# Kernel optimization log

Hardware: AMD Instinct MI355X
Metric: run time of the kernel (lower is better)

The kernel has to match this reference:

```python
import jax, jax.numpy as jnp
import numpy as np

N = 300000; E = N - 1; A = 150000; D = 64; H = 128; T = 512
NEG_SLOPE = 0.2


def _gatv2(h, src, dst, Wl, bl, Wr, br, att, bias):
    # PyG GATv2Conv, heads=1, add_self_loops=False
    xl = h @ Wl + bl            # source transform [N,H]
    xr = h @ Wr + br            # target transform [N,H]
    e = xl[src] + xr[dst]       # [E,H]
    a = jax.nn.leaky_relu(e, NEG_SLOPE) @ att   # [E]
    amax = jax.ops.segment_max(a, dst, num_segments=N)
    ex = jnp.exp(a - amax[dst])
    denom = jax.ops.segment_sum(ex, dst, num_segments=N)
    alpha = ex / (denom[dst] + 1e-16)
    out = jax.ops.segment_sum(alpha[:, None] * xl[src], dst, num_segments=N)
    return out + bias


def setup_inputs() -> dict:
    ks = jax.random.split(jax.random.key(0), 32)
    s = 0.02
    inp = {
        'x': jax.random.normal(ks[0], (N, D), jnp.float32),
        'edge_index': jax.random.randint(ks[1], (2, E), 0, N),
        'focal_seq': jax.random.normal(ks[2], (1, D), jnp.float32),
        'child_idx': jax.random.randint(ks[3], (A,), 0, N),
        'parent_idx': jax.random.randint(ks[4], (A,), 0, N + 1) - 1,  # include -1 (no parent)
        'time_idx': jax.random.randint(ks[5], (A,), 0, T),
        'W_embed': jax.random.normal(ks[6], (D, H)) * s, 'b_embed': jnp.zeros((H,)),
        'bu_Wl': jax.random.normal(ks[7], (H, H)) * s, 'bu_bl': jnp.zeros((H,)),
        'bu_Wr': jax.random.normal(ks[8], (H, H)) * s, 'bu_br': jnp.zeros((H,)),
        'bu_att': jax.random.normal(ks[9], (H,)) * s, 'bu_bias': jnp.zeros((H,)),
        'td_Wl': jax.random.normal(ks[10], (H, H)) * s, 'td_bl': jnp.zeros((H,)),
        'td_Wr': jax.random.normal(ks[11], (H, H)) * s, 'td_br': jnp.zeros((H,)),
        'td_att': jax.random.normal(ks[12], (H,)) * s, 'td_bias': jnp.zeros((H,)),
        'time_table': jax.random.normal(ks[13], (T, H)) * s,
        'W_comb': jax.random.normal(ks[14], (2 * H, H)) * s, 'b_comb': jnp.zeros((H,)),
        'W_a1': jax.random.normal(ks[15], (3 * H, H)) * s, 'b_a1': jnp.zeros((H,)),
        'W_a2': jax.random.normal(ks[16], (H, 1)) * s, 'b_a2': jnp.zeros((1,)),
        'W_seq': jax.random.normal(ks[17], (D, H)) * s, 'b_seq': jnp.zeros((H,)),
    }
    return inp


def reference(x, edge_index, focal_seq, child_idx, parent_idx, time_idx,
              W_embed, b_embed,
              bu_Wl, bu_bl, bu_Wr, bu_br, bu_att, bu_bias,
              td_Wl, td_bl, td_Wr, td_br, td_att, td_bias,
              time_table, W_comb, b_comb, W_a1, b_a1, W_a2, b_a2,
              W_seq, b_seq):
    h = x @ W_embed + b_embed                       # [N,H]
    # bottom-up pass: edge_index flipped -> src=row1, dst=row0
    h_bu = _gatv2(h, edge_index[1], edge_index[0], bu_Wl, bu_bl, bu_Wr, bu_br, bu_att, bu_bias)
    h = h + jax.nn.relu(h_bu)
    # top-down pass: src=row0, dst=row1
    h_td = _gatv2(h, edge_index[0], edge_index[1], td_Wl, td_bl, td_Wr, td_br, td_att, td_bias)
    h = h + jax.nn.relu(h_td)
    context = focal_seq @ W_seq + b_seq             # [1,H]
    h_child = h[child_idx]                          # [A,H]
    h_parent = jnp.where((parent_idx == -1)[:, None], 0.0, h[parent_idx])
    branch = jnp.concatenate([h_child, h_parent], axis=-1) @ W_comb + b_comb  # [A,H]
    t_emb = time_table[time_idx]                    # [A,H]
    combined = jnp.concatenate([branch, t_emb, jnp.broadcast_to(context, (branch.shape[0], context.shape[1]))], axis=-1)  # [A,3H]
    logits = jax.nn.relu(combined @ W_a1 + b_a1) @ W_a2 + b_a2  # [A,1]
    return logits
```

## Files before the change

### kernel.cpp

```cpp
#include <hip/hip_runtime.h>
#include <hip/hip_bf16.h>

#define NN 300000
#define EE 299999
#define AA 150000
#define DD 64
#define HH 128
#define TT 512
#define SCAN_NB ((NN + 1023) / 1024)

typedef unsigned short u16;
typedef unsigned int u32;
typedef __attribute__((ext_vector_type(8))) short short8;
typedef __attribute__((ext_vector_type(4))) float f32x4;

__device__ __forceinline__ float bfb(u16 u) { return __uint_as_float(((u32)u) << 16); }
__device__ __forceinline__ u16 f2b(float f) {
    u32 u = __float_as_uint(f);
    u32 r = (u + 0x7FFFu + ((u >> 16) & 1u)) >> 16;
    return (u16)r;
}
__device__ __forceinline__ uint4 load8(const u16* p) { return *(const uint4*)p; }
__device__ __forceinline__ uint4 load8(const float* p) {
    float4 f1 = *(const float4*)p;
    float4 f2 = *(const float4*)(p + 4);
    union { ushort s[8]; uint4 v; } u;
    u.s[0] = f2b(f1.x); u.s[1] = f2b(f1.y); u.s[2] = f2b(f1.z); u.s[3] = f2b(f1.w);
    u.s[4] = f2b(f2.x); u.s[5] = f2b(f2.y); u.s[6] = f2b(f2.z); u.s[7] = f2b(f2.w);
    return u.v;
}
__device__ __forceinline__ void unpack8(uint4 v, float* f) {
    u32 w0 = v.x, w1 = v.y, w2 = v.z, w3 = v.w;
    f[0] = bfb((u16)w0); f[1] = bfb((u16)(w0 >> 16));
    f[2] = bfb((u16)w1); f[3] = bfb((u16)(w1 >> 16));
    f[4] = bfb((u16)w2); f[5] = bfb((u16)(w2 >> 16));
    f[6] = bfb((u16)w3); f[7] = bfb((u16)(w3 >> 16));
}

__global__ __launch_bounds__(256) void k_wtrans(const float* w0, const float* w1,
                                                const float* w2, const float* w3,
                                                const float* w4, const float* w5,
                                                const float* w6, const float* w7,
                                                u16* __restrict__ wt) {
    int widx = blockIdx.x >> 3, part = blockIdx.x & 7;
    const float* W; int K = 128;
    switch (widx) {
        case 0: W = w0; break; case 1: W = w1; break;
        case 2: W = w2; break; case 3: W = w3; break;
        case 4: W = w4; break; case 5: W = w5; break;
        case 6: W = w6; break; default: W = w7; K = 64; break;
    }
    u16* dst = wt + widx * 16384;
    int total = K * 128;
    int lo = part * 2048, hi = lo + 2048;
    if (hi > total) hi = total;
    for (int idx = lo + threadIdx.x; idx < hi; idx += 256) {
        int k = idx >> 7, n = idx & 127;
        dst[n * K + k] = f2b(W[k * 128 + n]);
    }
}

__global__ void k_context(const float* __restrict__ focal, const float* __restrict__ Wseq,
                          const float* __restrict__ bseq, float* __restrict__ ctx) {
    int t = threadIdx.x;
    float acc = bseq[t];
    for (int d = 0; d < DD; ++d) acc = fmaf(focal[d], Wseq[d * HH + t], acc);
    ctx[t] = acc;
}

__global__ void k_c1(const float* __restrict__ ctx, const float* __restrict__ Wa1c,
                     const float* __restrict__ ba1, float* __restrict__ c1) {
    int t = threadIdx.x;
    float acc = ba1[t];
    for (int k = 0; k < HH; ++k) acc = fmaf(ctx[k], Wa1c[k * HH + t], acc);
    c1[t] = acc;
}

__global__ void k_tproj(const float* __restrict__ tt, const float* __restrict__ Wa1m,
                        float* __restrict__ tproj) {
    int ti = blockIdx.x, t = threadIdx.x;
    float acc = 0.f;
    for (int k = 0; k < HH; ++k)
        acc = fmaf(tt[ti * HH + k], Wa1m[k * HH + t], acc);
    tproj[(size_t)ti * HH + t] = acc;
}

__global__ void k_hist(const int* __restrict__ dst, int* __restrict__ counts) {
    int e = blockIdx.x * 256 + threadIdx.x;
    if (e < EE) atomicAdd(&counts[dst[e]], 1);
}

__global__ __launch_bounds__(256) void k_scan_block(const int* __restrict__ in,
                                                    int* __restrict__ out,
                                                    int* __restrict__ bsum, int n) {
    __shared__ int sh[256];
    int b = blockIdx.x, t = threadIdx.x;
    int base = b * 1024 + t * 4;
    int v0 = (base + 0 < n) ? in[base + 0] : 0;
    int v1 = (base + 1 < n) ? in[base + 1] : 0;
    int v2 = (base + 2 < n) ? in[base + 2] : 0;
    int v3 = (base + 3 < n) ? in[base + 3] : 0;
    int tsum = v0 + v1 + v2 + v3;
    sh[t] = tsum;
    __syncthreads();
    for (int d = 1; d < 256; d <<= 1) {
        int x = (t >= d) ? sh[t - d] : 0;
        __syncthreads();
        sh[t] += x;
        __syncthreads();
    }
    int excl = sh[t] - tsum;
    if (t == 255) bsum[b] = sh[255];
    if (base + 0 < n) out[base + 0] = excl;
    if (base + 1 < n) out[base + 1] = excl + v0;
    if (base + 2 < n) out[base + 2] = excl + v0 + v1;
    if (base + 3 < n) out[base + 3] = excl + v0 + v1 + v2;
}

__global__ __launch_bounds__(256) void k_scan_top(int* __restrict__ data, int n) {
    __shared__ int sh[256];
    int t = threadIdx.x;
    int base = t * 4;
    int v0 = (base + 0 < n) ? data[base + 0] : 0;
    int v1 = (base + 1 < n) ? data[base + 1] : 0;
    int v2 = (base + 2 < n) ? data[base + 2] : 0;
    int v3 = (base + 3 < n) ? data[base + 3] : 0;
    int tsum = v0 + v1 + v2 + v3;
    sh[t] = tsum;
    __syncthreads();
    for (int d = 1; d < 256; d <<= 1) {
        int x = (t >= d) ? sh[t - d] : 0;
        __syncthreads();
        sh[t] += x;
        __syncthreads();
    }
    int excl = sh[t] - tsum;
    if (base + 0 < n) data[base + 0] = excl;
    if (base + 1 < n) data[base + 1] = excl + v0;
    if (base + 2 < n) data[base + 2] = excl + v0 + v1;
    if (base + 3 < n) data[base + 3] = excl + v0 + v1 + v2;
}

__global__ void k_scan_add(int* __restrict__ out, const int* __restrict__ bsum, int n) {
    int i = blockIdx.x * 256 + threadIdx.x;
    if (i < n) out[i] += bsum[i >> 10];
}

__global__ void k_settail(int* o1, int* o2) {
    if (threadIdx.x == 0) { o1[NN] = EE; o2[NN] = EE; }
}

__global__ void k_scatter(const int* __restrict__ src, const int* __restrict__ dst,
                          int* __restrict__ cursor, int* __restrict__ elist) {
    int e = blockIdx.x * 256 + threadIdx.x;
    if (e >= EE) return;
    int pos = atomicAdd(&cursor[dst[e]], 1);
    elist[pos] = src[e];
}

template <int K, typename InT>
__global__ __launch_bounds__(256) void k_mfma_proj(const InT* __restrict__ in,
                                                   const u16* __restrict__ WT,
                                                   const float* __restrict__ bias,
                                                   u16* __restrict__ out, int nrows) {
    __shared__ u16 lds[2][128 * 72];
    u16* a_lds = lds[0];
    u16* b_lds = lds[1];
    u16* clds = lds[0];
    const int t = threadIdx.x;
    const int tile_m = blockIdx.x * 128;
    const int wave = t >> 6, l = t & 15, quad = (t >> 4) & 3;
    const int wr = wave >> 1, wc = wave & 1;
    f32x4 acc[4][4] = {};

    for (int chunk = 0; chunk < K / 64; ++chunk) {
        const int c0 = chunk * 64;
        __syncthreads();
        for (int ci = t; ci < 1024; ci += 256) {
            int row = ci >> 3, kc = ci & 7;
            int grow = tile_m + row;
            uint4 v = make_uint4(0, 0, 0, 0);
            if (grow < nrows) v = load8(&in[(size_t)grow * K + c0 + kc * 8]);
            *(uint4*)&a_lds[row * 72 + kc * 8] = v;
        }
        for (int ci = t; ci < 1024; ci += 256) {
            int n = ci >> 3, kc = ci & 7;
            *(uint4*)&b_lds[n * 72 + kc * 8] = *(const uint4*)&WT[(size_t)n * K + c0 + kc * 8];
        }
        __syncthreads();
#pragma unroll
        for (int ks = 0; ks < 2; ++ks) {
            short8 af[4], bf[4];
#pragma unroll
            for (int i = 0; i < 4; ++i)
                af[i] = *(const short8*)&a_lds[(wr * 64 + i * 16 + l) * 72 + ks * 32 + quad * 8];
#pragma unroll
            for (int j = 0; j < 4; ++j)
                bf[j] = *(const short8*)&b_lds[(wc * 64 + j * 16 + l) * 72 + ks * 32 + quad * 8];
#pragma unroll
            for (int i = 0; i < 4; ++i)
#pragma unroll
                for (int j = 0; j < 4; ++j)
                    acc[i][j] = __builtin_amdgcn_mfma_f32_16x16x32_bf16(af[i], bf[j], acc[i][j], 0, 0, 0);
        }
    }
    __syncthreads();
#pragma unroll
    for (int j = 0; j < 4; ++j) {
        int col = wc * 64 + j * 16 + l;
        float b = bias[col];
#pragma unroll
        for (int i = 0; i < 4; ++i) {
            int rloc = wr * 64 + i * 16 + quad * 4;
#pragma unroll
            for (int r = 0; r < 4; ++r)
                clds[(rloc + r) * 136 + col] = f2b(acc[i][j][r] + b);
        }
    }
    __syncthreads();
#pragma unroll
    for (int it = 0; it < 8; ++it) {
        int idx = it * 256 + t;
        int row = idx >> 4, c16 = idx & 15;
        int grow = tile_m + row;
        if (grow < nrows)
            *(uint4*)&out[(size_t)grow * HH + c16 * 8] = *(const uint4*)&clds[row * 136 + c16 * 8];
    }
}

__global__ __launch_bounds__(256) void k_mfma_gproj(const u16* __restrict__ h,
                                                    const int* __restrict__ idx1,
                                                    const int* __restrict__ idx2,
                                                    const u16* __restrict__ WT1,
                                                    const u16* __restrict__ WT2,
                                                    const float* __restrict__ bias,
                                                    u16* __restrict__ out, int nrows) {
    __shared__ u16 lds[2][128 * 72];
    u16* a_lds = lds[0];
    u16* b_lds = lds[1];
    u16* clds = lds[0];
    const int t = threadIdx.x;
    const int tile_m = blockIdx.x * 128;
    const int wave = t >> 6, l = t & 15, quad = (t >> 4) & 3;
    const int wr = wave >> 1, wc = wave & 1;
    f32x4 acc[4][4] = {};

    for (int pass = 0; pass < 2; ++pass) {
        const int* idx = pass ? idx2 : idx1;
        const u16* WT = pass ? WT2 : WT1;
        for (int chunk = 0; chunk < 2; ++chunk) {
            const int c0 = chunk * 64;
            __syncthreads();
            for (int ci = t; ci < 1024; ci += 256) {
                int row = ci >> 3, kc = ci & 7;
                int item = tile_m + row;
                int g = (item < nrows) ? idx[item] : -1;
                uint4 v = make_uint4(0, 0, 0, 0);
                if (g >= 0) v = load8(&h[(size_t)g * HH + c0 + kc * 8]);
                *(uint4*)&a_lds[row * 72 + kc * 8] = v;
            }
            for (int ci = t; ci < 1024; ci += 256) {
                int n = ci >> 3, kc = ci & 7;
                *(uint4*)&b_lds[n * 72 + kc * 8] = *(const uint4*)&WT[(size_t)n * HH + c0 + kc * 8];
            }
            __syncthreads();
#pragma unroll
            for (int ks = 0; ks < 2; ++ks) {
                short8 af[4], bf[4];
#pragma unroll
                for (int i = 0; i < 4; ++i)
                    af[i] = *(const short8*)&a_lds[(wr * 64 + i * 16 + l) * 72 + ks * 32 + quad * 8];
#pragma unroll
                for (int j = 0; j < 4; ++j)
                    bf[j] = *(const short8*)&b_lds[(wc * 64 + j * 16 + l) * 72 + ks * 32 + quad * 8];
#pragma unroll
                for (int i = 0; i < 4; ++i)
#pragma unroll
                    for (int j = 0; j < 4; ++j)
                        acc[i][j] = __builtin_amdgcn_mfma_f32_16x16x32_bf16(af[i], bf[j], acc[i][j], 0, 0, 0);
            }
        }
    }
    __syncthreads();
#pragma unroll
    for (int j = 0; j < 4; ++j) {
        int col = wc * 64 + j * 16 + l;
        float b = bias[col];
#pragma unroll
        for (int i = 0; i < 4; ++i) {
            int rloc = wr * 64 + i * 16 + quad * 4;
#pragma unroll
            for (int r = 0; r < 4; ++r)
                clds[(rloc + r) * 136 + col] = f2b(acc[i][j][r] + b);
        }
    }
    __syncthreads();
#pragma unroll
    for (int it = 0; it < 8; ++it) {
        int idx = it * 256 + t;
        int row = idx >> 4, c16 = idx & 15;
        int item = tile_m + row;
        if (item < nrows)
            *(uint4*)&out[(size_t)item * HH + c16 * 8] = *(const uint4*)&clds[row * 136 + c16 * 8];
    }
}

__global__ __launch_bounds__(256) void k_mfma_zlogit(const u16* __restrict__ branch,
                                                     const int* __restrict__ time_idx,
                                                     const float* __restrict__ tproj,
                                                     const float* __restrict__ c1,
                                                     const u16* __restrict__ WTa1,
                                                     const float* __restrict__ Wa2,
                                                     const float* __restrict__ ba2,
                                                     float* __restrict__ out) {
    __shared__ u16 a_lds[128 * 72];
    __shared__ u16 b_lds[128 * 72];
    __shared__ float red[2][128];
    const int t = threadIdx.x;
    const int tile_m = blockIdx.x * 128;
    const int wave = t >> 6, l = t & 15, quad = (t >> 4) & 3;
    const int wr = wave >> 1, wc = wave & 1;
    f32x4 acc[4][4] = {};

    for (int chunk = 0; chunk < 2; ++chunk) {
        const int c0 = chunk * 64;
        __syncthreads();
        for (int ci = t; ci < 1024; ci += 256) {
            int row = ci >> 3, kc = ci & 7;
            int item = tile_m + row;
            uint4 v = make_uint4(0, 0, 0, 0);
            if (item < AA) v = load8(&branch[(size_t)item * HH + c0 + kc * 8]);
            *(uint4*)&a_lds[row * 72 + kc * 8] = v;
        }
        for (int ci = t; ci < 1024; ci += 256) {
            int n = ci >> 3, kc = ci & 7;
            *(uint4*)&b_lds[n * 72 + kc * 8] = *(const uint4*)&WTa1[(size_t)n * HH + c0 + kc * 8];
        }
        __syncthreads();
#pragma unroll
        for (int ks = 0; ks < 2; ++ks) {
            short8 af[4], bf[4];
#pragma unroll
            for (int i = 0; i < 4; ++i)
                af[i] = *(const short8*)&a_lds[(wr * 64 + i * 16 + l) * 72 + ks * 32 + quad * 8];
#pragma unroll
            for (int j = 0; j < 4; ++j)
                bf[j] = *(const short8*)&b_lds[(wc * 64 + j * 16 + l) * 72 + ks * 32 + quad * 8];
#pragma unroll
            for (int i = 0; i < 4; ++i)
#pragma unroll
                for (int j = 0; j < 4; ++j)
                    acc[i][j] = __builtin_amdgcn_mfma_f32_16x16x32_bf16(af[i], bf[j], acc[i][j], 0, 0, 0);
        }
    }
    float c1v[4], wa2v[4];
#pragma unroll
    for (int j = 0; j < 4; ++j) {
        int col = wc * 64 + j * 16 + l;
        c1v[j] = c1[col];
        wa2v[j] = Wa2[col];
    }
#pragma unroll
    for (int i = 0; i < 4; ++i) {
        int rbase = tile_m + wr * 64 + i * 16 + quad * 4;
#pragma unroll
        for (int r = 0; r < 4; ++r) {
            int item = rbase + r;
            int ti = (item < AA) ? time_idx[item] : 0;
            const float* tp = tproj + (size_t)ti * HH;
            float partial = 0.f;
#pragma unroll
            for (int j = 0; j < 4; ++j) {
                int col = wc * 64 + j * 16 + l;
                float z = fmaxf(acc[i][j][r] + tp[col] + c1v[j], 0.f);
                partial = fmaf(z, wa2v[j], partial);
            }
            partial += __shfl_xor(partial, 1);
            partial += __shfl_xor(partial, 2);
            partial += __shfl_xor(partial, 4);
            partial += __shfl_xor(partial, 8);
            if (l == 0) red[wc][wr * 64 + i * 16 + quad * 4 + r] = partial;
        }
    }
    __syncthreads();
    if (t < 128) {
        int item = tile_m + t;
        if (item < AA) out[item] = red[0][t] + red[1][t] + ba2[0];
    }
}

__global__ __launch_bounds__(256) void k_gat_fused(u16* __restrict__ h,
                                                   const u16* __restrict__ xl,
                                                   const u16* __restrict__ xr,
                                                   const int* __restrict__ offs,
                                                   const int* __restrict__ elist,
                                                   const float* __restrict__ att,
                                                   const float* __restrict__ bias) {
    int g = blockIdx.x * 16 + (threadIdx.x >> 4);
    int l = threadIdx.x & 15;
    float attv[8], biasv[8];
    *(float4*)&attv[0] = *(const float4*)&att[l * 8];
    *(float4*)&attv[4] = *(const float4*)&att[l * 8 + 4];
    *(float4*)&biasv[0] = *(const float4*)&bias[l * 8];
    *(float4*)&biasv[4] = *(const float4*)&bias[l * 8 + 4];
    float xrf[8];
    unpack8(*(const uint4*)&xr[(size_t)g * HH + l * 8], xrf);
    int e0 = offs[g], e1 = offs[g + 1];

    float m = -__builtin_inff(), s = 0.f;
    for (int e = e0; e < e1; ++e) {
        int sidx = elist[e];
        float xf[8];
        unpack8(*(const uint4*)&xl[(size_t)sidx * HH + l * 8], xf);
        float p = 0.f;
#pragma unroll
        for (int j = 0; j < 8; ++j) {
            float v = xf[j] + xrf[j];
            v = v >= 0.f ? v : 0.2f * v;
            p = fmaf(v, attv[j], p);
        }
        p += __shfl_xor(p, 1); p += __shfl_xor(p, 2);
        p += __shfl_xor(p, 4); p += __shfl_xor(p, 8);
        float mn = fmaxf(m, p);
        s = s * __expf(m - mn) + __expf(p - mn);
        m = mn;
    }
    float inv = 1.f / (s + 1e-16f);

    float acc[8] = {};
    for (int e = e0; e < e1; ++e) {
        int sidx = elist[e];
        float xf[8];
        unpack8(*(const uint4*)&xl[(size_t)sidx * HH + l * 8], xf);
        float p = 0.f;
#pragma unroll
        for (int j = 0; j < 8; ++j) {
            float v = xf[j] + xrf[j];
            v = v >= 0.f ? v : 0.2f * v;
            p = fmaf(v, attv[j], p);
        }
        p += __shfl_xor(p, 1); p += __shfl_xor(p, 2);
        p += __shfl_xor(p, 4); p += __shfl_xor(p, 8);
        float w = __expf(p - m) * inv;
#pragma unroll
        for (int j = 0; j < 8; ++j) acc[j] = fmaf(w, xf[j], acc[j]);
    }

    float hf[8];
    unpack8(*(const uint4*)&h[(size_t)g * HH + l * 8], hf);
    union { ushort sh[8]; uint4 v; } o;
#pragma unroll
    for (int j = 0; j < 8; ++j) {
        hf[j] += fmaxf(acc[j] + biasv[j], 0.f);
        o.sh[j] = f2b(hf[j]);
    }
    *(uint4*)&h[(size_t)g * HH + l * 8] = o.v;
}

typedef const float* fp;

static void build_csr(const int* src, const int* dst, int* offs, int* elist,
                      int* work , int* bsum, hipStream_t stream) {
    hipMemsetAsync(work, 0, (size_t)NN * 4, stream);
    k_hist<<<(EE + 255) / 256, 256, 0, stream>>>(dst, work);
    k_scan_block<<<SCAN_NB, 256, 0, stream>>>(work, offs, bsum, NN);
    k_scan_top<<<1, 256, 0, stream>>>(bsum, SCAN_NB);
    k_scan_add<<<(NN + 255) / 256, 256, 0, stream>>>(offs, bsum, NN);
    hipMemcpyAsync(work, offs, (size_t)NN * 4, hipMemcpyDeviceToDevice, stream);
    k_scatter<<<(EE + 255) / 256, 256, 0, stream>>>(src, dst, work, elist);
}

extern "C" void kernel_launch(void* const* d_in, const int* in_sizes, int n_in,
                              void* d_out, int out_size, void* d_ws, size_t ws_size,
                              hipStream_t stream) {
    fp x                 = (fp)d_in[0];
    const int* ei        = (const int*)d_in[1];
    fp focal             = (fp)d_in[2];
    const int* child_idx = (const int*)d_in[3];
    const int* parent_idx= (const int*)d_in[4];
    const int* time_idx  = (const int*)d_in[5];
    fp W_embed = (fp)d_in[6],  b_embed = (fp)d_in[7];
    fp bu_Wl   = (fp)d_in[8],  bu_bl   = (fp)d_in[9];
    fp bu_Wr   = (fp)d_in[10], bu_br   = (fp)d_in[11];
    fp bu_att  = (fp)d_in[12], bu_bias = (fp)d_in[13];
    fp td_Wl   = (fp)d_in[14], td_bl   = (fp)d_in[15];
    fp td_Wr   = (fp)d_in[16], td_br   = (fp)d_in[17];
    fp td_att  = (fp)d_in[18], td_bias = (fp)d_in[19];
    fp time_table = (fp)d_in[20];
    fp W_comb  = (fp)d_in[21], b_comb  = (fp)d_in[22];
    fp W_a1    = (fp)d_in[23], b_a1    = (fp)d_in[24];
    fp W_a2    = (fp)d_in[25], b_a2    = (fp)d_in[26];
    fp W_seq   = (fp)d_in[27], b_seq   = (fp)d_in[28];

    const size_t NH = (size_t)NN * HH;
    u16* wt = (u16*)d_ws;
    u16* h  = wt + 8 * 16384;
    u16* xl = h + NH;
    u16* xr = xl + NH;
    u16* branch = xl;
    float* ctx   = (float*)(xr + NH);
    float* c1v   = ctx + HH;
    float* tproj = c1v + HH;
    int* offsBU  = (int*)(tproj + (size_t)TT * HH);
    int* offsTD  = offsBU + NN + 1;
    int* elistBU = offsTD + NN + 1;
    int* elistTD = elistBU + EE;
    int* csr_work= elistTD + EE;
    int* bsum    = csr_work + NN;

    build_csr(ei + EE, ei, offsBU, elistBU, csr_work, bsum, stream);
    build_csr(ei, ei + EE, offsTD, elistTD, csr_work, bsum, stream);
    k_settail<<<1, 64, 0, stream>>>(offsBU, offsTD);

    k_wtrans<<<64, 256, 0, stream>>>(bu_Wl, bu_Wr, td_Wl, td_Wr,
                                     W_comb, W_comb + (size_t)HH * HH, W_a1, W_embed, wt);
    const u16* wt_buWl = wt + 0 * 16384;
    const u16* wt_buWr = wt + 1 * 16384;
    const u16* wt_tdWl = wt + 2 * 16384;
    const u16* wt_tdWr = wt + 3 * 16384;
    const u16* wt_combC = wt + 4 * 16384;
    const u16* wt_combP = wt + 5 * 16384;
    const u16* wt_a1   = wt + 6 * 16384;
    const u16* wt_embed = wt + 7 * 16384;

    k_context<<<1, 128, 0, stream>>>(focal, W_seq, b_seq, ctx);
    k_c1<<<1, 128, 0, stream>>>(ctx, W_a1 + (size_t)256 * HH, b_a1, c1v);
    k_tproj<<<TT, 128, 0, stream>>>(time_table, W_a1 + (size_t)128 * HH, tproj);

    const int NB = (NN + 127) / 128;
    k_mfma_proj<64, float><<<NB, 256, 0, stream>>>(x, wt_embed, b_embed, h, NN);

    k_mfma_proj<128, u16><<<NB, 256, 0, stream>>>(h, wt_buWl, bu_bl, xl, NN);
    k_mfma_proj<128, u16><<<NB, 256, 0, stream>>>(h, wt_buWr, bu_br, xr, NN);
    k_gat_fused<<<NN / 16, 256, 0, stream>>>(h, xl, xr, offsBU, elistBU, bu_att, bu_bias);

    k_mfma_proj<128, u16><<<NB, 256, 0, stream>>>(h, wt_tdWl, td_bl, xl, NN);
    k_mfma_proj<128, u16><<<NB, 256, 0, stream>>>(h, wt_tdWr, td_br, xr, NN);
    k_gat_fused<<<NN / 16, 256, 0, stream>>>(h, xl, xr, offsTD, elistTD, td_att, td_bias);

    k_mfma_gproj<<<(AA + 127) / 128, 256, 0, stream>>>(
        h, child_idx, parent_idx, wt_combC, wt_combP, b_comb, branch, AA);

    k_mfma_zlogit<<<(AA + 127) / 128, 256, 0, stream>>>(
        branch, time_idx, tproj, c1v, wt_a1, W_a2, b_a2, (float*)d_out);
}
```

Measured before the change: 665.6 us.

## Fuse Wl/Wr projections into one kernel and use single-pass online softmax in GAT

Adds a dual-output MFMA projection kernel that loads each tile of h once and computes both the source and target transforms, replacing two separate projection launches per GAT layer. The GAT aggregation kernel now folds the softmax max/sum and the weighted accumulation into one online-softmax pass over the edges. That halves the gathers of xl rows per destination node. In exchange the projection kernel uses more LDS and accumulator registers, which can lower occupancy, and the online rescaling adds an extra exp per edge.

```diff
diff --git a/kernel.cpp b/kernel.cpp
--- a/kernel.cpp
+++ b/kernel.cpp
@@ -225,6 +225,106 @@
         int grow = tile_m + row;
         if (grow < nrows)
             *(uint4*)&out[(size_t)grow * HH + c16 * 8] = *(const uint4*)&clds[row * 136 + c16 * 8];
+    }
+}
+
+__global__ __launch_bounds__(256) void k_mfma_proj2(const u16* __restrict__ in,
+                                                    const u16* __restrict__ WT1,
+                                                    const u16* __restrict__ WT2,
+                                                    const float* __restrict__ b1,
+                                                    const float* __restrict__ b2,
+                                                    u16* __restrict__ out1,
+                                                    u16* __restrict__ out2, int nrows) {
+    __shared__ u16 lds[3 * 128 * 72];
+    u16* a_lds = lds;
+    u16* b1_lds = lds + 128 * 72;
+    u16* b2_lds = lds + 2 * 128 * 72;
+    u16* clds = lds;
+    const int t = threadIdx.x;
+    const int tile_m = blockIdx.x * 128;
+    const int wave = t >> 6, l = t & 15, quad = (t >> 4) & 3;
+    const int wr = wave >> 1, wc = wave & 1;
+    f32x4 acc1[4][4] = {}, acc2[4][4] = {};
+
+    for (int chunk = 0; chunk < 2; ++chunk) {
+        const int c0 = chunk * 64;
+        __syncthreads();
+        for (int ci = t; ci < 1024; ci += 256) {
+            int row = ci >> 3, kc = ci & 7;
+            int grow = tile_m + row;
+            uint4 v = make_uint4(0, 0, 0, 0);
+            if (grow < nrows) v = load8(&in[(size_t)grow * HH + c0 + kc * 8]);
+            *(uint4*)&a_lds[row * 72 + kc * 8] = v;
+        }
+        for (int ci = t; ci < 1024; ci += 256) {
+            int n = ci >> 3, kc = ci & 7;
+            *(uint4*)&b1_lds[n * 72 + kc * 8] = *(const uint4*)&WT1[(size_t)n * HH + c0 + kc * 8];
+            *(uint4*)&b2_lds[n * 72 + kc * 8] = *(const uint4*)&WT2[(size_t)n * HH + c0 + kc * 8];
+        }
+        __syncthreads();
+#pragma unroll
+        for (int ks = 0; ks < 2; ++ks) {
+            short8 af[4], bf1[4], bf2[4];
+#pragma unroll
+            for (int i = 0; i < 4; ++i)
+                af[i] = *(const short8*)&a_lds[(wr * 64 + i * 16 + l) * 72 + ks * 32 + quad * 8];
+#pragma unroll
+            for (int j = 0; j < 4; ++j) {
+                bf1[j] = *(const short8*)&b1_lds[(wc * 64 + j * 16 + l) * 72 + ks * 32 + quad * 8];
+                bf2[j] = *(const short8*)&b2_lds[(wc * 64 + j * 16 + l) * 72 + ks * 32 + quad * 8];
+            }
+#pragma unroll
+            for (int i = 0; i < 4; ++i)
+#pragma unroll
+                for (int j = 0; j < 4; ++j) {
+                    acc1[i][j] = __builtin_amdgcn_mfma_f32_16x16x32_bf16(af[i], bf1[j], acc1[i][j], 0, 0, 0);
+                    acc2[i][j] = __builtin_amdgcn_mfma_f32_16x16x32_bf16(af[i], bf2[j], acc2[i][j], 0, 0, 0);
+                }
+        }
+    }
+    __syncthreads();
+#pragma unroll
+    for (int j = 0; j < 4; ++j) {
+        int col = wc * 64 + j * 16 + l;
+        float b = b1[col];
+#pragma unroll
+        for (int i = 0; i < 4; ++i) {
+            int rloc = wr * 64 + i * 16 + quad * 4;
+#pragma unroll
+            for (int r = 0; r < 4; ++r)
+                clds[(rloc + r) * 136 + col] = f2b(acc1[i][j][r] + b);
+        }
+    }
+    __syncthreads();
+#pragma unroll
+    for (int it = 0; it < 8; ++it) {
+        int idx = it * 256 + t;
+        int row = idx >> 4, c16 = idx & 15;
+        int grow = tile_m + row;
+        if (grow < nrows)
+            *(uint4*)&out1[(size_t)grow * HH + c16 * 8] = *(const uint4*)&clds[row * 136 + c16 * 8];
+    }
+    __syncthreads();
+#pragma unroll
+    for (int j = 0; j < 4; ++j) {
+        int col = wc * 64 + j * 16 + l;
+        float b = b2[col];
+#pragma unroll
+        for (int i = 0; i < 4; ++i) {
+            int rloc = wr * 64 + i * 16 + quad * 4;
+#pragma unroll
+            for (int r = 0; r < 4; ++r)
+                clds[(rloc + r) * 136 + col] = f2b(acc2[i][j][r] + b);
+        }
+    }
+    __syncthreads();
+#pragma unroll
+    for (int it = 0; it < 8; ++it) {
+        int idx = it * 256 + t;
+        int row = idx >> 4, c16 = idx & 15;
+        int grow = tile_m + row;
+        if (grow < nrows)
+            *(uint4*)&out2[(size_t)grow * HH + c16 * 8] = *(const uint4*)&clds[row * 136 + c16 * 8];
     }
 }
 
@@ -408,25 +508,6 @@
     int e0 = offs[g], e1 = offs[g + 1];
 
     float m = -__builtin_inff(), s = 0.f;
-    for (int e = e0; e < e1; ++e) {
-        int sidx = elist[e];
-        float xf[8];
-        unpack8(*(const uint4*)&xl[(size_t)sidx * HH + l * 8], xf);
-        float p = 0.f;
-#pragma unroll
-        for (int j = 0; j < 8; ++j) {
-            float v = xf[j] + xrf[j];
-            v = v >= 0.f ? v : 0.2f * v;
-            p = fmaf(v, attv[j], p);
-        }
-        p += __shfl_xor(p, 1); p += __shfl_xor(p, 2);
-        p += __shfl_xor(p, 4); p += __shfl_xor(p, 8);
-        float mn = fmaxf(m, p);
-        s = s * __expf(m - mn) + __expf(p - mn);
-        m = mn;
-    }
-    float inv = 1.f / (s + 1e-16f);
-
     float acc[8] = {};
     for (int e = e0; e < e1; ++e) {
         int sidx = elist[e];
@@ -441,17 +522,22 @@
         }
         p += __shfl_xor(p, 1); p += __shfl_xor(p, 2);
         p += __shfl_xor(p, 4); p += __shfl_xor(p, 8);
-        float w = __expf(p - m) * inv;
-#pragma unroll
-        for (int j = 0; j < 8; ++j) acc[j] = fmaf(w, xf[j], acc[j]);
-    }
+        float mn = fmaxf(m, p);
+        float so = __expf(m - mn);
+        float w = __expf(p - mn);
+        s = s * so + w;
+#pragma unroll
+        for (int j = 0; j < 8; ++j) acc[j] = fmaf(acc[j], so, w * xf[j]);
+        m = mn;
+    }
+    float inv = 1.f / (s + 1e-16f);
 
     float hf[8];
     unpack8(*(const uint4*)&h[(size_t)g * HH + l * 8], hf);
     union { ushort sh[8]; uint4 v; } o;
 #pragma unroll
     for (int j = 0; j < 8; ++j) {
-        hf[j] += fmaxf(acc[j] + biasv[j], 0.f);
+        hf[j] += fmaxf(fmaf(acc[j], inv, biasv[j]), 0.f);
         o.sh[j] = f2b(hf[j]);
     }
     *(uint4*)&h[(size_t)g * HH + l * 8] = o.v;
@@ -460,7 +546,7 @@
 typedef const float* fp;
 
 static void build_csr(const int* src, const int* dst, int* offs, int* elist,
-                      int* work , int* bsum, hipStream_t stream) {
+                      int* work, int* bsum, hipStream_t stream) {
     hipMemsetAsync(work, 0, (size_t)NN * 4, stream);
     k_hist<<<(EE + 255) / 256, 256, 0, stream>>>(dst, work);
     k_scan_block<<<SCAN_NB, 256, 0, stream>>>(work, offs, bsum, NN);
@@ -530,12 +616,10 @@
     const int NB = (NN + 127) / 128;
     k_mfma_proj<64, float><<<NB, 256, 0, stream>>>(x, wt_embed, b_embed, h, NN);
 
-    k_mfma_proj<128, u16><<<NB, 256, 0, stream>>>(h, wt_buWl, bu_bl, xl, NN);
-    k_mfma_proj<128, u16><<<NB, 256, 0, stream>>>(h, wt_buWr, bu_br, xr, NN);
+    k_mfma_proj2<<<NB, 256, 0, stream>>>(h, wt_buWl, wt_buWr, bu_bl, bu_br, xl, xr, NN);
     k_gat_fused<<<NN / 16, 256, 0, stream>>>(h, xl, xr, offsBU, elistBU, bu_att, bu_bias);
 
-    k_mfma_proj<128, u16><<<NB, 256, 0, stream>>>(h, wt_tdWl, td_bl, xl, NN);
-    k_mfma_proj<128, u16><<<NB, 256, 0, stream>>>(h, wt_tdWr, td_br, xr, NN);
+    k_mfma_proj2<<<NB, 256, 0, stream>>>(h, wt_tdWl, wt_tdWr, td_bl, td_br, xl, xr, NN);
     k_gat_fused<<<NN / 16, 256, 0, stream>>>(h, xl, xr, offsTD, elistTD, td_att, td_bias);
 
     k_mfma_gproj<<<(AA + 127) / 128, 256, 0, stream>>>(
```

After: 633.2 us. 1.05x faster.
